# Performance work log

Measured on AMD Instinct MI355X. Metric: run time of the kernel, lower is better.

## Reference

```python
import jax, jax.numpy as jnp
import numpy as np

N = 100000   # num nodes
E = 3200000  # num edges (avg degree 32)
H = 64       # hidden_dim
EPS = 1e-5   # batchnorm eps


def setup_inputs() -> dict:
    key = jax.random.key(0)
    ks = jax.random.split(key, 12)
    def gl(k, shp):  # glorot-ish init
        fan = shp[0]
        return jax.random.normal(k, shp, dtype=jnp.float32) / np.sqrt(fan)
    return dict(
        x=jax.random.normal(ks[0], (N, 4), dtype=jnp.float32),
        src=jax.random.randint(ks[1], (E,), 0, N, dtype=jnp.int32),
        dst=jax.random.randint(ks[2], (E,), 0, N, dtype=jnp.int32),
        W0=gl(ks[3], (4, H)), b0=jnp.zeros((H,), jnp.float32),
        W1=gl(ks[4], (H, H)), b1=jnp.zeros((H,), jnp.float32),
        g0=jnp.ones((H,), jnp.float32), be0=jnp.zeros((H,), jnp.float32),
        g1=jnp.ones((H,), jnp.float32), be1=jnp.zeros((H,), jnp.float32),
        Wm0=gl(ks[5], (H, H)), bm0=jnp.zeros((H,), jnp.float32),
        Wm1=gl(ks[6], (H, H // 2)), bm1=jnp.zeros((H // 2,), jnp.float32),
        Wm2=gl(ks[7], (H // 2, 1)), bm2=jnp.zeros((1,), jnp.float32),
    )


def gcn_conv(x, W, b, src, dst, n):
    # PyG GCNConv: add self-loops, symmetric D^-1/2 (A+I) D^-1/2 normalization,
    # linear transform, scatter-add aggregation at destination, then bias.
    h = x @ W                                   # [n, out]
    loop = jnp.arange(n, dtype=src.dtype)
    s = jnp.concatenate([src, loop])            # sources incl self-loops
    d = jnp.concatenate([dst, loop])            # targets incl self-loops
    deg = jax.ops.segment_sum(jnp.ones_like(d, dtype=h.dtype), d, num_segments=n)
    dinv = jnp.where(deg > 0, jax.lax.rsqrt(deg), 0.0)
    norm = dinv[s] * dinv[d]                    # [E+n]
    msg = h[s] * norm[:, None]                  # gather + scale
    out = jax.ops.segment_sum(msg, d, num_segments=n)  # scatter-add
    return out + b


def batchnorm(x, g, b):
    # training-mode BatchNorm1d over the node dimension (biased variance)
    mu = jnp.mean(x, axis=0)
    var = jnp.mean(jnp.square(x - mu), axis=0)
    return g * (x - mu) * jax.lax.rsqrt(var + EPS) + b


def reference(x, src, dst, W0, b0, W1, b1, g0, be0, g1, be1,
              Wm0, bm0, Wm1, bm1, Wm2, bm2):
    n = x.shape[0]
    h = gcn_conv(x, W0, b0, src, dst, n)
    h = jax.nn.relu(batchnorm(h, g0, be0))      # dropout = identity (eval)
    h = gcn_conv(h, W1, b1, src, dst, n)
    h = jax.nn.relu(batchnorm(h, g1, be1))
    h = jax.nn.relu(h @ Wm0 + bm0)
    h = jax.nn.relu(h @ Wm1 + bm1)
    return jax.nn.sigmoid(h @ Wm2 + bm2)        # [n, 1] collision probs
```

## Files before the change

kernel.cpp:

```cpp
#include <hip/hip_runtime.h>
#include <hip/hip_fp16.h>
#include <math.h>

#define HD 64
#define EPS 1e-5f
#define BSH 9
#define BSZ 512
#define T1 16384
#define BCAP 20480

__device__ __forceinline__ float atomAddF(float* p, float v) {
    return unsafeAtomicAdd(p, v);
}


__global__ void k_ginit(int* __restrict__ gcur) {
    int t = threadIdx.x;
    gcur[t] = t * BCAP;
}

__global__ __launch_bounds__(256) void k_bucket(const int* __restrict__ src,
        const int* __restrict__ dst, int* __restrict__ gcur,
        unsigned* __restrict__ bedges, int e) {
    __shared__ int hist[256];
    __shared__ int base[256];
    int t = threadIdx.x;
    for (int tile = blockIdx.x * T1; tile < e; tile += gridDim.x * T1) {
        int lim = min(e - tile, T1);
        hist[t] = 0;
        __syncthreads();
        for (int j = t; j < lim; j += 256)
            atomicAdd(&hist[dst[tile + j] >> BSH], 1);
        __syncthreads();
        int h = hist[t];
        int mybase = (h > 0) ? atomicAdd(&gcur[t], h) : 0;
        __syncthreads();
        hist[t] = 0;
        base[t] = mybase;
        __syncthreads();
        for (int j = t; j < lim; j += 256) {
            int d = dst[tile + j], s = src[tile + j];
            int bk = d >> BSH;
            int loc = atomicAdd(&hist[bk], 1);
            bedges[base[bk] + loc] = ((unsigned)(d & (BSZ - 1)) << 17) | (unsigned)s;
        }
        __syncthreads();
    }
}

__global__ __launch_bounds__(256) void k_bscan(const int* __restrict__ gcur,
        int* __restrict__ boff, int* __restrict__ row_ptr, int nb, int n, int e) {
    __shared__ int sc[256];
    int t = threadIdx.x;
    int v = (t < nb) ? (gcur[t] - t * BCAP) : 0;
    sc[t] = v;
    __syncthreads();
    int acc = v;
    for (int off = 1; off < 256; off <<= 1) {
        int x = (t >= off) ? sc[t - off] : 0;
        __syncthreads();
        acc += x;
        sc[t] = acc;
        __syncthreads();
    }
    boff[t] = acc - v;
    if (t == 0) row_ptr[n] = e;
}

__global__ __launch_bounds__(256) void k_build(const unsigned* __restrict__ bedges,
        const int* __restrict__ boff, int* __restrict__ row_ptr,
        unsigned* __restrict__ csr, float* __restrict__ dinv, int n) {
    __shared__ int hist[BSZ];
    __shared__ int cur[BSZ];
    __shared__ int sc[256];
    int b = blockIdx.x, t = threadIdx.x;
    int nodebase = b << BSH;
    int cbase = boff[b];
    int cnt = boff[b + 1] - cbase;
    const unsigned* bed = bedges + (size_t)b * BCAP;
    hist[t] = 0; hist[t + 256] = 0;
    __syncthreads();
    for (int j = t; j < cnt; j += 256)
        atomicAdd(&hist[bed[j] >> 17], 1);
    __syncthreads();
    int a0 = hist[2 * t], a1 = hist[2 * t + 1];
    int psum = a0 + a1;
    sc[t] = psum;
    __syncthreads();
    int acc = psum;
    for (int off = 1; off < 256; off <<= 1) {
        int x = (t >= off) ? sc[t - off] : 0;
        __syncthreads();
        acc += x;
        sc[t] = acc;
        __syncthreads();
    }
    int excl = acc - psum;
    int e0 = cbase + excl, e1 = cbase + excl + a0;
    cur[2 * t] = e0;
    cur[2 * t + 1] = e1;
    int n0 = nodebase + 2 * t, n1 = nodebase + 2 * t + 1;
    if (n0 < n) { row_ptr[n0] = e0; dinv[n0] = rsqrtf((float)(a0 + 1)); }
    if (n1 < n) { row_ptr[n1] = e1; dinv[n1] = rsqrtf((float)(a1 + 1)); }
    __syncthreads();
    for (int j = t; j < cnt; j += 256) {
        unsigned p = bed[j];
        int pos = atomicAdd(&cur[p >> 17], 1);
        csr[pos] = p;
    }
}


__global__ __launch_bounds__(256) void k_lin0(const float* __restrict__ x,
        const float* __restrict__ W0, const float* __restrict__ dinv,
        __half* __restrict__ A, int n_nodes) {
    __shared__ float w[4 * HD];
    int t = threadIdx.x;
    w[t] = W0[t];
    __syncthreads();
    int n = blockIdx.x * 4 + (t >> 6);
    int c = t & 63;
    if (n >= n_nodes) return;
    float x0 = x[n * 4 + 0], x1 = x[n * 4 + 1], x2 = x[n * 4 + 2], x3 = x[n * 4 + 3];
    float v = x0 * w[c] + x1 * w[64 + c] + x2 * w[128 + c] + x3 * w[192 + c];
    A[((size_t)n << 6) + c] = __float2half(v * dinv[n]);
}

__global__ __launch_bounds__(256) void k_aggr(const int* __restrict__ row_ptr,
        const unsigned* __restrict__ pedges, const __half* __restrict__ A,
        const float* __restrict__ dinv, const float* __restrict__ bias,
        float* __restrict__ B, float* __restrict__ stats, int n_nodes) {
    __shared__ float acc[64 * 65];
    __shared__ float ls[4][64], ls2[4][64];
    int t = threadIdx.x;
    for (int i = t; i < 64 * 65; i += 256) acc[i] = 0.f;
    int nodebase = blockIdx.x << 6;
    int nend = min(nodebase + 64, n_nodes);
    int ebeg = row_ptr[nodebase];
    int eend = row_ptr[nend];
    int nedges = eend - ebeg;
    __syncthreads();

    int wv = t >> 6, lane = t & 63;
    int sub = lane >> 4, ch = lane & 15;
    int s = wv * 4 + sub;
    int sbeg = ebeg + (int)(((long long)nedges * s) >> 4);
    int send = ebeg + (int)(((long long)nedges * (s + 1)) >> 4);
    const uint2* A2 = (const uint2*)A;

    float a0 = 0.f, a1 = 0.f, a2 = 0.f, a3 = 0.f;
    int cur = -1;

    #define FLUSH() if (cur >= 0) {                                            \
        int o_ = cur * 65 + (ch << 2);                                         \
        atomicAdd(&acc[o_ + 0], a0); atomicAdd(&acc[o_ + 1], a1);              \
        atomicAdd(&acc[o_ + 2], a2); atomicAdd(&acc[o_ + 3], a3); }

    #define PROC(P, U) {                                                       \
        int d_ = (int)((P) >> 17) & 63;                                        \
        if (d_ != cur) { FLUSH(); a0 = a1 = a2 = a3 = 0.f; cur = d_; }         \
        float2 f01_ = __half22float2(*(const __half2*)&(U).x);                 \
        float2 f23_ = __half22float2(*(const __half2*)&(U).y);                 \
        a0 += f01_.x; a1 += f01_.y; a2 += f23_.x; a3 += f23_.y; }

    int j = sbeg;
    for (; j + 16 <= send; j += 16) {
        unsigned p[16];
        uint2 u[16];
        #pragma unroll
        for (int k = 0; k < 16; ++k) p[k] = pedges[j + k];
        #pragma unroll
        for (int k = 0; k < 16; ++k)
            u[k] = A2[(((size_t)(p[k] & 0x1FFFFu)) << 4) + ch];
        #pragma unroll
        for (int k = 0; k < 16; ++k) PROC(p[k], u[k]);
    }
    for (; j < send; ++j) {
        unsigned p0 = pedges[j];
        uint2 u0 = A2[(((size_t)(p0 & 0x1FFFFu)) << 4) + ch];
        PROC(p0, u0);
    }
    FLUSH();
    #undef PROC
    #undef FLUSH
    __syncthreads();

    int c = lane;
    float st = 0.f, st2 = 0.f;
    for (int r = wv; r < 64; r += 4) {
        int node = nodebase + r;
        if (node < n_nodes) {
            float v = acc[r * 65 + c] + __half2float(A[((size_t)node << 6) + c]);
            v = dinv[node] * v + bias[c];
            B[((size_t)node << 6) + c] = v;
            st += v; st2 += v * v;
        }
    }
    ls[wv][c] = st; ls2[wv][c] = st2;
    __syncthreads();
    if (t < 64) {
        atomAddF(&stats[t], ls[0][t] + ls[1][t] + ls[2][t] + ls[3][t]);
        atomAddF(&stats[64 + t], ls2[0][t] + ls2[1][t] + ls2[2][t] + ls2[3][t]);
    }
}

__global__ __launch_bounds__(256) void k_lin1(const float* __restrict__ B,
        const float* __restrict__ W, const float* __restrict__ dinv,
        const float* __restrict__ stats, const float* __restrict__ g,
        const float* __restrict__ be, __half* __restrict__ A, int n_nodes) {
    __shared__ float w[HD * HD];
    __shared__ float rows[4][HD];
    int t = threadIdx.x;
    for (int i = t; i < HD * HD; i += 256) w[i] = W[i];
    int wv = t >> 6, c = t & 63;
    float inv_n = 1.0f / (float)n_nodes;
    float mu = stats[c] * inv_n;
    float var = stats[64 + c] * inv_n - mu * mu;
    float sc = g[c] * rsqrtf(var + EPS);
    float sh = be[c] - mu * sc;
    int ngroups = (n_nodes + 3) >> 2;
    for (int gidx = blockIdx.x; gidx < ngroups; gidx += gridDim.x) {
        __syncthreads();
        int n = gidx * 4 + wv;
        float rv = (n < n_nodes) ? fmaxf(sc * B[((size_t)n << 6) + c] + sh, 0.f) : 0.f;
        rows[wv][c] = rv;
        __syncthreads();
        if (n < n_nodes) {
            float acc = 0.f;
            #pragma unroll
            for (int k = 0; k < HD; k++) acc = fmaf(rows[wv][k], w[k * 64 + c], acc);
            A[((size_t)n << 6) + c] = __float2half(acc * dinv[n]);
        }
    }
}

__global__ __launch_bounds__(256) void k_mlp(const float* __restrict__ B,
        const float* __restrict__ stats, const float* __restrict__ g,
        const float* __restrict__ be,
        const float* __restrict__ Wm0, const float* __restrict__ bm0,
        const float* __restrict__ Wm1, const float* __restrict__ bm1,
        const float* __restrict__ Wm2, const float* __restrict__ bm2,
        float* __restrict__ out, int n_nodes) {
    __shared__ float rows[32][66];
    __shared__ float scb[64], shb[64];
    int t = threadIdx.x;
    if (t < 64) {
        float inv_n = 1.0f / (float)n_nodes;
        float mu = stats[t] * inv_n;
        float var = stats[64 + t] * inv_n - mu * mu;
        float sc = g[t] * rsqrtf(var + EPS);
        scb[t] = sc;
        shb[t] = be[t] - mu * sc;
    }
    __syncthreads();
    int nbase = blockIdx.x * 32;
    #pragma unroll 8
    for (int i = 0; i < 8; ++i) {
        int idx = t + i * 256;
        int r = idx >> 6, c = idx & 63;
        int nn = nbase + r;
        float v = (nn < n_nodes) ? B[((size_t)nn << 6) + c] : 0.f;
        rows[r][c] = fmaxf(scb[c] * v + shb[c], 0.f);
    }
    __syncthreads();

    int w = t >> 6, j = t & 63;
    int rb = w * 8;
    float acc0[8];
    float b0j = bm0[j];
    #pragma unroll
    for (int i = 0; i < 8; ++i) acc0[i] = b0j;
    #pragma unroll 4
    for (int k = 0; k < 64; k += 2) {
        float wv0 = Wm0[k * 64 + j];
        float wv1 = Wm0[(k + 1) * 64 + j];
        #pragma unroll
        for (int i = 0; i < 8; ++i) {
            float2 hv = *(const float2*)&rows[rb + i][k];
            acc0[i] = fmaf(hv.x, wv0, acc0[i]);
            acc0[i] = fmaf(hv.y, wv1, acc0[i]);
        }
    }
    #pragma unroll
    for (int i = 0; i < 8; ++i) rows[rb + i][j] = fmaxf(acc0[i], 0.f);
    __syncthreads();
    int h = j >> 5, ch2 = j & 31;
    int rb1 = rb + h * 4;
    float acc2[4];
    float b1j = bm1[ch2];
    #pragma unroll
    for (int i = 0; i < 4; ++i) acc2[i] = b1j;
    #pragma unroll 4
    for (int k = 0; k < 64; k += 2) {
        float wv0 = Wm1[k * 32 + ch2];
        float wv1 = Wm1[(k + 1) * 32 + ch2];
        #pragma unroll
        for (int i = 0; i < 4; ++i) {
            float2 hv = *(const float2*)&rows[rb1 + i][k];
            acc2[i] = fmaf(hv.x, wv0, acc2[i]);
            acc2[i] = fmaf(hv.y, wv1, acc2[i]);
        }
    }
    float wm2 = Wm2[ch2];
    float z[4];
    #pragma unroll
    for (int i = 0; i < 4; ++i) z[i] = fmaxf(acc2[i], 0.f) * wm2;
    #pragma unroll
    for (int d = 1; d < 32; d <<= 1) {
        #pragma unroll
        for (int i = 0; i < 4; ++i) z[i] += __shfl_xor(z[i], d, 64);
    }
    if (ch2 == 0) {
        float bb = bm2[0];
        #pragma unroll
        for (int i = 0; i < 4; ++i) {
            int nn = nbase + rb1 + i;
            if (nn < n_nodes)
                out[nn] = 1.0f / (1.0f + __expf(-(z[i] + bb)));
        }
    }
}

extern "C" void kernel_launch(void* const* d_in, const int* in_sizes, int n_in,
                              void* d_out, int out_size, void* d_ws, size_t ws_size,
                              hipStream_t stream) {
    const float* x   = (const float*)d_in[0];
    const int*   src = (const int*)d_in[1];
    const int*   dst = (const int*)d_in[2];
    const float* W0  = (const float*)d_in[3];
    const float* b0  = (const float*)d_in[4];
    const float* W1  = (const float*)d_in[5];
    const float* b1  = (const float*)d_in[6];
    const float* g0  = (const float*)d_in[7];
    const float* be0 = (const float*)d_in[8];
    const float* g1  = (const float*)d_in[9];
    const float* be1 = (const float*)d_in[10];
    const float* Wm0 = (const float*)d_in[11];
    const float* bm0 = (const float*)d_in[12];
    const float* Wm1 = (const float*)d_in[13];
    const float* bm1 = (const float*)d_in[14];
    const float* Wm2 = (const float*)d_in[15];
    const float* bm2 = (const float*)d_in[16];

    int n = in_sizes[0] / 4;
    int e = in_sizes[1];
    float* out = (float*)d_out;

    int nb = (n + BSZ - 1) >> BSH;

    char* ws = (char*)d_ws;
    auto alignup = [](size_t v) { return (v + 255) & ~(size_t)255; };
    size_t o = 0;
    int*      boff    = (int*)(ws + o);      o += alignup(257 * 4);
    int*      gcur    = (int*)(ws + o);      o += alignup(256 * 4);
    float*    stats   = (float*)(ws + o);    o += alignup(256 * 4);
    int*      row_ptr = (int*)(ws + o);      o += alignup((size_t)(n + 1) * 4);
    float*    dinv    = (float*)(ws + o);    o += alignup((size_t)n * 4);
    unsigned* bedges  = (unsigned*)(ws + o); o += alignup((size_t)nb * BCAP * 4);
    unsigned* csr     = (unsigned*)(ws + o); o += alignup((size_t)e * 4);
    __half*   A       = (__half*)(ws + o);   o += alignup((size_t)n * 64 * 2);
    float*    B       = (float*)(ws + o);

    int gN4    = (n + 3) / 4;
    int ntiles = (e + T1 - 1) / T1;
    int gMLP   = (n + 31) / 32;
    int gAGG   = (n + 63) / 64;

    (void)hipMemsetAsync(stats, 0, 256 * 4, stream);

    k_ginit<<<1, 256, 0, stream>>>(gcur);
    k_bucket<<<ntiles, 256, 0, stream>>>(src, dst, gcur, bedges, e);
    k_bscan<<<1, 256, 0, stream>>>(gcur, boff, row_ptr, nb, n, e);
    k_build<<<nb, 256, 0, stream>>>(bedges, boff, row_ptr, csr, dinv, n);

    k_lin0<<<gN4, 256, 0, stream>>>(x, W0, dinv, A, n);
    k_aggr<<<gAGG, 256, 0, stream>>>(row_ptr, csr, A, dinv, b0, B, stats, n);

    k_lin1<<<2048, 256, 0, stream>>>(B, W1, dinv, stats, g0, be0, A, n);
    k_aggr<<<gAGG, 256, 0, stream>>>(row_ptr, csr, A, dinv, b1, B, stats + 128, n);

    k_mlp<<<gMLP, 256, 0, stream>>>(B, stats + 128, g1, be1,
                                    Wm0, bm0, Wm1, bm1, Wm2, bm2, out, n);
}
```

Baseline: 369.5 us.

## Use smaller buckets and tiles with vectorized loads in CSR build

Halves the bucket size to 256 nodes, giving about 391 buckets, and shrinks bucketing tiles to 4096 edges so more blocks run with one tile each. Edges are held in registers after int4 vector loads, so the second pass does not re-read them. The build kernel now maps one node per thread and reads the bucket list with uint4 loads. This targets the CSR construction phase by raising parallelism, at the cost of more global atomics on gcur and a larger scan.

```diff
diff --git a/kernel.cpp b/kernel.cpp
--- a/kernel.cpp
+++ b/kernel.cpp
@@ -4,59 +4,85 @@
 
 #define HD 64
 #define EPS 1e-5f
-#define BSH 9
-#define BSZ 512
-#define T1 16384
-#define BCAP 20480
+#define BSH 8
+#define BSZ 256
+#define T1 4096
+#define BCAP 10240
 
 __device__ __forceinline__ float atomAddF(float* p, float v) {
     return unsafeAtomicAdd(p, v);
 }
 
 
-__global__ void k_ginit(int* __restrict__ gcur) {
+__global__ __launch_bounds__(512) void k_ginit(int* __restrict__ gcur) {
     int t = threadIdx.x;
     gcur[t] = t * BCAP;
 }
 
 __global__ __launch_bounds__(256) void k_bucket(const int* __restrict__ src,
         const int* __restrict__ dst, int* __restrict__ gcur,
-        unsigned* __restrict__ bedges, int e) {
-    __shared__ int hist[256];
-    __shared__ int base[256];
-    int t = threadIdx.x;
-    for (int tile = blockIdx.x * T1; tile < e; tile += gridDim.x * T1) {
-        int lim = min(e - tile, T1);
-        hist[t] = 0;
-        __syncthreads();
+        unsigned* __restrict__ bedges, int e, int nbuck) {
+    __shared__ int hist[512];
+    __shared__ int base[512];
+    int t = threadIdx.x;
+    int tile = blockIdx.x * T1;
+    int lim = min(e - tile, T1);
+    hist[t] = 0; hist[t + 256] = 0;
+    __syncthreads();
+    int d_[16], s_[16];
+    bool full = (lim == T1);
+    if (full) {
+        const int4* d4 = (const int4*)(dst + tile);
+        const int4* s4 = (const int4*)(src + tile);
+        #pragma unroll
+        for (int j = 0; j < 4; ++j) {
+            int4 dv = d4[j * 256 + t];
+            int4 sv = s4[j * 256 + t];
+            d_[4 * j + 0] = dv.x; d_[4 * j + 1] = dv.y;
+            d_[4 * j + 2] = dv.z; d_[4 * j + 3] = dv.w;
+            s_[4 * j + 0] = sv.x; s_[4 * j + 1] = sv.y;
+            s_[4 * j + 2] = sv.z; s_[4 * j + 3] = sv.w;
+        }
+        #pragma unroll
+        for (int j = 0; j < 16; ++j) atomicAdd(&hist[d_[j] >> BSH], 1);
+    } else {
         for (int j = t; j < lim; j += 256)
             atomicAdd(&hist[dst[tile + j] >> BSH], 1);
-        __syncthreads();
-        int h = hist[t];
-        int mybase = (h > 0) ? atomicAdd(&gcur[t], h) : 0;
-        __syncthreads();
-        hist[t] = 0;
-        base[t] = mybase;
-        __syncthreads();
+    }
+    __syncthreads();
+    for (int b = t; b < nbuck; b += 256) {
+        int h = hist[b];
+        base[b] = (h > 0) ? atomicAdd(&gcur[b], h) : 0;
+        hist[b] = 0;
+    }
+    __syncthreads();
+    if (full) {
+        #pragma unroll
+        for (int j = 0; j < 16; ++j) {
+            int bk = d_[j] >> BSH;
+            int loc = atomicAdd(&hist[bk], 1);
+            bedges[base[bk] + loc] =
+                ((unsigned)(d_[j] & (BSZ - 1)) << 17) | (unsigned)s_[j];
+        }
+    } else {
         for (int j = t; j < lim; j += 256) {
             int d = dst[tile + j], s = src[tile + j];
             int bk = d >> BSH;
             int loc = atomicAdd(&hist[bk], 1);
             bedges[base[bk] + loc] = ((unsigned)(d & (BSZ - 1)) << 17) | (unsigned)s;
         }
-        __syncthreads();
-    }
-}
-
-__global__ __launch_bounds__(256) void k_bscan(const int* __restrict__ gcur,
+    }
+}
+
+__global__ __launch_bounds__(512) void k_bscan(const int* __restrict__ gcur,
         int* __restrict__ boff, int* __restrict__ row_ptr, int nb, int n, int e) {
-    __shared__ int sc[256];
+    __shared__ int sc[512];
     int t = threadIdx.x;
     int v = (t < nb) ? (gcur[t] - t * BCAP) : 0;
     sc[t] = v;
     __syncthreads();
     int acc = v;
-    for (int off = 1; off < 256; off <<= 1) {
+    for (int off = 1; off < 512; off <<= 1) {
         int x = (t >= off) ? sc[t - off] : 0;
         __syncthreads();
         acc += x;
@@ -78,16 +104,21 @@
     int cbase = boff[b];
     int cnt = boff[b + 1] - cbase;
     const unsigned* bed = bedges + (size_t)b * BCAP;
-    hist[t] = 0; hist[t + 256] = 0;
-    __syncthreads();
-    for (int j = t; j < cnt; j += 256)
-        atomicAdd(&hist[bed[j] >> 17], 1);
-    __syncthreads();
-    int a0 = hist[2 * t], a1 = hist[2 * t + 1];
-    int psum = a0 + a1;
-    sc[t] = psum;
-    __syncthreads();
-    int acc = psum;
+    hist[t] = 0;
+    __syncthreads();
+    int cnt4 = cnt & ~3;
+    for (int jj = t * 4; jj < cnt4; jj += 1024) {
+        uint4 p = *(const uint4*)(bed + jj);
+        atomicAdd(&hist[p.x >> 17], 1); atomicAdd(&hist[p.y >> 17], 1);
+        atomicAdd(&hist[p.z >> 17], 1); atomicAdd(&hist[p.w >> 17], 1);
+    }
+    for (int jj = cnt4 + t; jj < cnt; jj += 256)
+        atomicAdd(&hist[bed[jj] >> 17], 1);
+    __syncthreads();
+    int a = hist[t];
+    sc[t] = a;
+    __syncthreads();
+    int acc = a;
     for (int off = 1; off < 256; off <<= 1) {
         int x = (t >= off) ? sc[t - off] : 0;
         __syncthreads();
@@ -95,16 +126,20 @@
         sc[t] = acc;
         __syncthreads();
     }
-    int excl = acc - psum;
-    int e0 = cbase + excl, e1 = cbase + excl + a0;
-    cur[2 * t] = e0;
-    cur[2 * t + 1] = e1;
-    int n0 = nodebase + 2 * t, n1 = nodebase + 2 * t + 1;
-    if (n0 < n) { row_ptr[n0] = e0; dinv[n0] = rsqrtf((float)(a0 + 1)); }
-    if (n1 < n) { row_ptr[n1] = e1; dinv[n1] = rsqrtf((float)(a1 + 1)); }
-    __syncthreads();
-    for (int j = t; j < cnt; j += 256) {
-        unsigned p = bed[j];
+    int e0 = cbase + acc - a;
+    cur[t] = e0;
+    int node = nodebase + t;
+    if (node < n) { row_ptr[node] = e0; dinv[node] = rsqrtf((float)(a + 1)); }
+    __syncthreads();
+    for (int jj = t * 4; jj < cnt4; jj += 1024) {
+        uint4 p = *(const uint4*)(bed + jj);
+        int p0 = atomicAdd(&cur[p.x >> 17], 1); csr[p0] = p.x;
+        int p1 = atomicAdd(&cur[p.y >> 17], 1); csr[p1] = p.y;
+        int p2 = atomicAdd(&cur[p.z >> 17], 1); csr[p2] = p.z;
+        int p3 = atomicAdd(&cur[p.w >> 17], 1); csr[p3] = p.w;
+    }
+    for (int jj = cnt4 + t; jj < cnt; jj += 256) {
+        unsigned p = bed[jj];
         int pos = atomicAdd(&cur[p >> 17], 1);
         csr[pos] = p;
     }
@@ -351,8 +386,8 @@
     char* ws = (char*)d_ws;
     auto alignup = [](size_t v) { return (v + 255) & ~(size_t)255; };
     size_t o = 0;
-    int*      boff    = (int*)(ws + o);      o += alignup(257 * 4);
-    int*      gcur    = (int*)(ws + o);      o += alignup(256 * 4);
+    int*      boff    = (int*)(ws + o);      o += alignup(513 * 4);
+    int*      gcur    = (int*)(ws + o);      o += alignup(512 * 4);
     float*    stats   = (float*)(ws + o);    o += alignup(256 * 4);
     int*      row_ptr = (int*)(ws + o);      o += alignup((size_t)(n + 1) * 4);
     float*    dinv    = (float*)(ws + o);    o += alignup((size_t)n * 4);
@@ -368,9 +403,9 @@
 
     (void)hipMemsetAsync(stats, 0, 256 * 4, stream);
 
-    k_ginit<<<1, 256, 0, stream>>>(gcur);
-    k_bucket<<<ntiles, 256, 0, stream>>>(src, dst, gcur, bedges, e);
-    k_bscan<<<1, 256, 0, stream>>>(gcur, boff, row_ptr, nb, n, e);
+    k_ginit<<<1, 512, 0, stream>>>(gcur);
+    k_bucket<<<ntiles, 256, 0, stream>>>(src, dst, gcur, bedges, e, nb);
+    k_bscan<<<1, 512, 0, stream>>>(gcur, boff, row_ptr, nb, n, e);
     k_build<<<nb, 256, 0, stream>>>(bedges, boff, row_ptr, csr, dinv, n);
 
     k_lin0<<<gN4, 256, 0, stream>>>(x, W0, dinv, A, n);
```

Measured after the change: 334.9 us. -9.4%, faster.
